# Performance work log

Hardware: AMD Instinct MI355X
Metric: run time of the kernel (lower is better)

## Reference

```python
import jax, jax.numpy as jnp
import numpy as np

B = 2048   # batch of manifold points
D = 16     # manifold_dim


def setup_inputs() -> dict:
    key = jax.random.key(0)
    k1, k2 = jax.random.split(key)
    a = jax.random.normal(k1, (B, D, D), dtype=jnp.float32)
    # SPD, well-conditioned metric so the inverse in scalar_curvature is stable
    metric = jnp.einsum('bij,bkj->bik', a, a) / D + jnp.eye(D, dtype=jnp.float32)
    christoffel = jax.random.normal(k2, (B, D, D, D), dtype=jnp.float32) * 0.1
    return {"metric": metric, "christoffel": christoffel}


def reference(metric, christoffel):
    # --- riemann_curvature (fully vectorized; replaces dim^4 python loops) ---
    # torch.roll(christoffel[:, i, j, x], 1, dims=0) - christoffel[:, i, j, x]
    dG = jnp.roll(christoffel, 1, axis=0) - christoffel          # [B, i, j, x]
    partial_k = dG[:, :, :, None, :]                             # broadcast over k, indexed by l
    partial_l = dG[:, :, :, :, None]                             # broadcast over l, indexed by k
    # conn1[b,i,j,k,l] = sum_m Gamma[b,i,m,k] * Gamma[b,m,j,l]
    conn1 = jnp.einsum('bimk,bmjl->bijkl', christoffel, christoffel)
    # conn2[b,i,j,k,l] = sum_m Gamma[b,i,m,l] * Gamma[b,m,j,k]
    conn2 = jnp.einsum('biml,bmjk->bijkl', christoffel, christoffel)
    riemann = partial_k - partial_l + conn1 - conn2              # [B, D, D, D, D]

    # --- ricci_curvature: contraction 'bkikj->bij' ---
    ricci = jnp.einsum('bkikj->bij', riemann)                    # [B, D, D]

    # --- scalar_curvature: R = g^{ij} Ric_{ij} ---
    metric_inv = jnp.linalg.inv(metric)
    scalar = jnp.einsum('bij,bij->b', ricci, metric_inv)         # [B]
    return scalar
```

## Files before the change

kernel.cpp:

```cpp
#include <hip/hip_runtime.h>
#include <hip/hip_bf16.h>

#define NB 2048

typedef __attribute__((ext_vector_type(8))) short bf16x8;
typedef __attribute__((ext_vector_type(4))) float f32x4;

__device__ __forceinline__ float qget(const float4& q, int c) {
    return c == 0 ? q.x : c == 1 ? q.y : c == 2 ? q.z : q.w;
}

template<int CTRL>
__device__ __forceinline__ float dpp_mov(float x) {
    union { float f; int i; } u; u.f = x;
    u.i = __builtin_amdgcn_mov_dpp(u.i, CTRL, 0xf, 0xf, true);
    return u.f;
}
#define ROWSUM16(x) { x += dpp_mov<0x111>(x); x += dpp_mov<0x112>(x); \
                      x += dpp_mov<0x114>(x); x += dpp_mov<0x118>(x); }

#define GJ_STEP(K) { \
    constexpr int kq = (K) >> 2, kc = (K) & 3; \
    float akc = (kc == 0) ? a0 : (kc == 1) ? a1 : (kc == 2) ? a2 : a3; \
    union { float f; int i; } ua_, uf_, up_; \
    ua_.f = akc; \
    up_.i = __builtin_amdgcn_readlane(ua_.i, ((K) << 2) | kq); \
    uf_.i = __builtin_amdgcn_mov_dpp(ua_.i, kq * 0x55, 0xf, 0xf, 0); \
    float pv = up_.f; \
    float f  = uf_.f; \
    float q0 = __shfl(a0, ((K) << 2) | gq2); \
    float q1 = __shfl(a1, ((K) << 2) | gq2); \
    float q2 = __shfl(a2, ((K) << 2) | gq2); \
    float q3 = __shfl(a3, ((K) << 2) | gq2); \
    float pinv = 1.0f / pv; \
    bool piv = (gi == (K)); \
    float r0 = q0 * pinv, r1 = q1 * pinv, r2 = q2 * pinv, r3 = q3 * pinv; \
    a0 = piv ? r0 : fmaf(-f, r0, a0); \
    a1 = piv ? r1 : fmaf(-f, r1, a1); \
    a2 = piv ? r2 : fmaf(-f, r2, a2); \
    a3 = piv ? r3 : fmaf(-f, r3, a3); \
    float colv = piv ? pinv : -f * pinv; \
    bool fix = (gq2 == kq); \
    if      (kc == 0) a0 = fix ? colv : a0; \
    else if (kc == 1) a1 = fix ? colv : a1; \
    else if (kc == 2) a2 = fix ? colv : a2; \
    else              a3 = fix ? colv : a3; \
}

__global__ __launch_bounds__(256, 6)
void curvature_kernel(const float* __restrict__ metric,
                      const float* __restrict__ gamma,
                      float* __restrict__ out)
{
    const int bid = blockIdx.x;
    const int b = ((bid & 7) << 8) | (bid >> 3);
    const int t = threadIdx.x;
    const int wv = t >> 6, lane = t & 63;
    const int ku = t >> 4, iu = t & 15;
    const int r16 = lane & 15, hi = lane >> 4;
    const int gjw = b & 3;

    __shared__ alignas(16) unsigned short XA[16][264];
    __shared__ alignas(16) float MINV[16][20];
    __shared__ alignas(16) float TT[16][20];
    __shared__ float red[4];

    const float* Gc = gamma + ((size_t)b << 12);
    const float* Gp = gamma + ((size_t)((b + NB - 1) & (NB - 1)) << 12);
    const float4* gc4 = (const float4*)(Gc + (t << 4));
    const float4* gp4 = (const float4*)(Gp + (t << 4));
    const bool isGJ = (wv == gjw);

    float4 g0 = gc4[0], g1 = gc4[1], g2 = gc4[2], g3 = gc4[3];
    float4 mrow = {0.f, 0.f, 0.f, 0.f};
    if (isGJ) mrow = ((const float4*)(metric + ((size_t)b << 8)))[lane];

    float gku;
    {
        float4 gq[4] = {g0, g1, g2, g3};
        gku = g0.x;
        #pragma unroll
        for (int k = 1; k < 16; ++k) {
            float v = qget(gq[k >> 2], k & 3);
            gku = (ku == k) ? v : gku;
        }
    }

    if (isGJ) {
        const int gi = lane >> 2, gq2 = lane & 3;
        float a0 = mrow.x, a1 = mrow.y, a2 = mrow.z, a3 = mrow.w;
        GJ_STEP(0)  GJ_STEP(1)  GJ_STEP(2)  GJ_STEP(3)
        GJ_STEP(4)  GJ_STEP(5)  GJ_STEP(6)  GJ_STEP(7)
        GJ_STEP(8)  GJ_STEP(9)  GJ_STEP(10) GJ_STEP(11)
        GJ_STEP(12) GJ_STEP(13) GJ_STEP(14) GJ_STEP(15)
        MINV[gi][4*gq2 + 0] = a0;
        MINV[gi][4*gq2 + 1] = a1;
        MINV[gi][4*gq2 + 2] = a2;
        MINV[gi][4*gq2 + 3] = a3;
    }

    {
        float4 gq[4] = {g0, g1, g2, g3};
        unsigned yp[8];
        #pragma unroll
        for (int q = 0; q < 8; ++q) {
            union { __hip_bfloat162 h; unsigned u; } cv;
            cv.h = __float22bfloat162_rn(
                make_float2(qget(gq[q >> 1], (q & 1) * 2),
                            qget(gq[q >> 1], (q & 1) * 2 + 1)));
            yp[q] = cv.u;
        }
        uint4* xd = (uint4*)&XA[iu][ku << 4];
        xd[0] = make_uint4(yp[0], yp[1], yp[2], yp[3]);
        xd[1] = make_uint4(yp[4], yp[5], yp[6], yp[7]);
    }
    TT[iu][ku] = gku;
    __syncthreads();

    float4 m0, m1, m2, m3;
    {
        const float4* mv = (const float4*)&MINV[iu][0];
        m0 = mv[0]; m1 = mv[1]; m2 = mv[2]; m3 = mv[3];
    }

    f32x4 acc = {0.f, 0.f, 0.f, 0.f};
    #pragma unroll
    for (int s = 0; s < 2; ++s) {
        const int S = 2 * wv + s;
        bf16x8 av = *(const bf16x8*)&XA[r16][(S << 5) + (hi << 3)];
        const int brow = 2 * S + (hi >> 1);
        const int cbase = ((hi & 1) << 7) + r16;
        bf16x8 bv;
        #pragma unroll
        for (int e = 0; e < 8; ++e)
            bv[e] = (short)XA[brow][cbase + (e << 4)];
        acc = __builtin_amdgcn_mfma_f32_16x16x32_bf16(av, bv, acc, 0, 0, 0);
    }

    float pd = 0.f, pku = 0.f;
    {
        float4 v0 = gp4[0], v1 = gp4[1], v2 = gp4[2], v3 = gp4[3];
        float4 vq[4] = {v0, v1, v2, v3};
        #pragma unroll
        for (int k = 0; k < 16; ++k) {
            float v = qget(vq[k >> 2], k & 3);
            float m = qget((k < 4) ? m0 : (k < 8) ? m1 : (k < 12) ? m2 : m3, k & 3);
            pd = fmaf(v, m, pd);
            pku = (ku == k) ? v : pku;
        }
    }

    float qd = 0.f, R = 0.f;
    {
        float4 gq[4] = {g0, g1, g2, g3};
        #pragma unroll
        for (int k = 0; k < 16; ++k) {
            float m = qget((k < 4) ? m0 : (k < 8) ? m1 : (k < 12) ? m2 : m3, k & 3);
            qd = fmaf(qget(gq[k >> 2], k & 3), m, qd);
            R += m;
        }
    }

    float tsum = TT[ku][iu];
    float qsum = qd;
    ROWSUM16(tsum)
    ROWSUM16(qsum)

    float dt = pku - gku;
    float4 mq = (hi == 0) ? m0 : (hi == 1) ? m1 : (hi == 2) ? m2 : m3;
    float t4c = acc[0] * mq.x + acc[1] * mq.y + acc[2] * mq.z + acc[3] * mq.w;

    float s = pd - dt * R - t4c;
    if (iu == 15) s = fmaf(tsum - 1.0f, qsum, s);

    ROWSUM16(s)
    s += dpp_mov<0x142>(s);
    s += dpp_mov<0x143>(s);
    if (lane == 63) red[wv] = s;
    __syncthreads();
    if (t == 0) out[b] = (red[0] + red[1]) + (red[2] + red[3]);
}

extern "C" void kernel_launch(void* const* d_in, const int* in_sizes, int n_in,
                              void* d_out, int out_size, void* d_ws, size_t ws_size,
                              hipStream_t stream) {
    const float* metric = (const float*)d_in[0];
    const float* gamma  = (const float*)d_in[1];
    float* out = (float*)d_out;
    curvature_kernel<<<NB, 256, 0, stream>>>(metric, gamma, out);
}
```

Measured before the change: 12.46 us.

## Scatter roll-derivative term to neighbor batch via atomics instead of reloading previous christoffel

Each block no longer reads the previous batch's 16 KB christoffel slice. Instead it inverts the next batch's metric in a second wavefront and computes that batch's derivative contribution from its own christoffel data, adding both partial sums to the output with atomicAdd. The output must now be zeroed with an extra memset launch. This removes half of the gamma traffic, at the cost of a second Gauss-Jordan inversion per block, atomic writes, and a memset that falls inside the timed region.

```diff
diff --git a/kernel.cpp b/kernel.cpp
--- a/kernel.cpp
+++ b/kernel.cpp
@@ -54,26 +54,28 @@
 {
     const int bid = blockIdx.x;
     const int b = ((bid & 7) << 8) | (bid >> 3);
+    const int bn = (b + 1) & (NB - 1);
     const int t = threadIdx.x;
     const int wv = t >> 6, lane = t & 63;
     const int ku = t >> 4, iu = t & 15;
     const int r16 = lane & 15, hi = lane >> 4;
-    const int gjw = b & 3;
+    const int gjw  = b & 3;
+    const int gjw2 = (gjw + 1) & 3;
 
     __shared__ alignas(16) unsigned short XA[16][264];
     __shared__ alignas(16) float MINV[16][20];
+    __shared__ alignas(16) float MINVN[16][20];
     __shared__ alignas(16) float TT[16][20];
-    __shared__ float red[4];
+    __shared__ float red[4], red2[4];
 
     const float* Gc = gamma + ((size_t)b << 12);
-    const float* Gp = gamma + ((size_t)((b + NB - 1) & (NB - 1)) << 12);
     const float4* gc4 = (const float4*)(Gc + (t << 4));
-    const float4* gp4 = (const float4*)(Gp + (t << 4));
-    const bool isGJ = (wv == gjw);
+    const bool isGJ1 = (wv == gjw), isGJ2 = (wv == gjw2);
 
     float4 g0 = gc4[0], g1 = gc4[1], g2 = gc4[2], g3 = gc4[3];
     float4 mrow = {0.f, 0.f, 0.f, 0.f};
-    if (isGJ) mrow = ((const float4*)(metric + ((size_t)b << 8)))[lane];
+    if (isGJ1) mrow = ((const float4*)(metric + ((size_t)b  << 8)))[lane];
+    if (isGJ2) mrow = ((const float4*)(metric + ((size_t)bn << 8)))[lane];
 
     float gku;
     {
@@ -86,17 +88,18 @@
         }
     }
 
-    if (isGJ) {
+    if (isGJ1 || isGJ2) {
+        float (*MDST)[20] = isGJ1 ? MINV : MINVN;
         const int gi = lane >> 2, gq2 = lane & 3;
         float a0 = mrow.x, a1 = mrow.y, a2 = mrow.z, a3 = mrow.w;
         GJ_STEP(0)  GJ_STEP(1)  GJ_STEP(2)  GJ_STEP(3)
         GJ_STEP(4)  GJ_STEP(5)  GJ_STEP(6)  GJ_STEP(7)
         GJ_STEP(8)  GJ_STEP(9)  GJ_STEP(10) GJ_STEP(11)
         GJ_STEP(12) GJ_STEP(13) GJ_STEP(14) GJ_STEP(15)
-        MINV[gi][4*gq2 + 0] = a0;
-        MINV[gi][4*gq2 + 1] = a1;
-        MINV[gi][4*gq2 + 2] = a2;
-        MINV[gi][4*gq2 + 3] = a3;
+        MDST[gi][4*gq2 + 0] = a0;
+        MDST[gi][4*gq2 + 1] = a1;
+        MDST[gi][4*gq2 + 2] = a2;
+        MDST[gi][4*gq2 + 3] = a3;
     }
 
     {
@@ -117,10 +120,12 @@
     TT[iu][ku] = gku;
     __syncthreads();
 
-    float4 m0, m1, m2, m3;
+    float4 m0, m1, m2, m3, n0, n1, n2, n3;
     {
         const float4* mv = (const float4*)&MINV[iu][0];
         m0 = mv[0]; m1 = mv[1]; m2 = mv[2]; m3 = mv[3];
+        const float4* nv = (const float4*)&MINVN[iu][0];
+        n0 = nv[0]; n1 = nv[1]; n2 = nv[2]; n3 = nv[3];
     }
 
     f32x4 acc = {0.f, 0.f, 0.f, 0.f};
@@ -137,27 +142,18 @@
         acc = __builtin_amdgcn_mfma_f32_16x16x32_bf16(av, bv, acc, 0, 0, 0);
     }
 
-    float pd = 0.f, pku = 0.f;
-    {
-        float4 v0 = gp4[0], v1 = gp4[1], v2 = gp4[2], v3 = gp4[3];
-        float4 vq[4] = {v0, v1, v2, v3};
-        #pragma unroll
-        for (int k = 0; k < 16; ++k) {
-            float v = qget(vq[k >> 2], k & 3);
-            float m = qget((k < 4) ? m0 : (k < 8) ? m1 : (k < 12) ? m2 : m3, k & 3);
-            pd = fmaf(v, m, pd);
-            pku = (ku == k) ? v : pku;
-        }
-    }
-
-    float qd = 0.f, R = 0.f;
+    float qd = 0.f, R = 0.f, pn = 0.f, Rn = 0.f;
     {
         float4 gq[4] = {g0, g1, g2, g3};
         #pragma unroll
         for (int k = 0; k < 16; ++k) {
+            float v = qget(gq[k >> 2], k & 3);
             float m = qget((k < 4) ? m0 : (k < 8) ? m1 : (k < 12) ? m2 : m3, k & 3);
-            qd = fmaf(qget(gq[k >> 2], k & 3), m, qd);
+            float n = qget((k < 4) ? n0 : (k < 8) ? n1 : (k < 12) ? n2 : n3, k & 3);
+            qd = fmaf(v, m, qd);
+            pn = fmaf(v, n, pn);
             R += m;
+            Rn += n;
         }
     }
 
@@ -166,19 +162,23 @@
     ROWSUM16(tsum)
     ROWSUM16(qsum)
 
-    float dt = pku - gku;
     float4 mq = (hi == 0) ? m0 : (hi == 1) ? m1 : (hi == 2) ? m2 : m3;
     float t4c = acc[0] * mq.x + acc[1] * mq.y + acc[2] * mq.z + acc[3] * mq.w;
 
-    float s = pd - dt * R - t4c;
+    float s = fmaf(gku, R, -t4c);
     if (iu == 15) s = fmaf(tsum - 1.0f, qsum, s);
+    float s2 = fmaf(-gku, Rn, pn);
 
     ROWSUM16(s)
-    s += dpp_mov<0x142>(s);
-    s += dpp_mov<0x143>(s);
-    if (lane == 63) red[wv] = s;
+    s += dpp_mov<0x142>(s);   s += dpp_mov<0x143>(s);
+    ROWSUM16(s2)
+    s2 += dpp_mov<0x142>(s2); s2 += dpp_mov<0x143>(s2);
+    if (lane == 63) { red[wv] = s; red2[wv] = s2; }
     __syncthreads();
-    if (t == 0) out[b] = (red[0] + red[1]) + (red[2] + red[3]);
+    if (t == 0) {
+        atomicAdd(&out[b],  (red[0]  + red[1])  + (red[2]  + red[3]));
+        atomicAdd(&out[bn], (red2[0] + red2[1]) + (red2[2] + red2[3]));
+    }
 }
 
 extern "C" void kernel_launch(void* const* d_in, const int* in_sizes, int n_in,
@@ -187,5 +187,6 @@
     const float* metric = (const float*)d_in[0];
     const float* gamma  = (const float*)d_in[1];
     float* out = (float*)d_out;
+    hipMemsetAsync(out, 0, (size_t)out_size * sizeof(float), stream);
     curvature_kernel<<<NB, 256, 0, stream>>>(metric, gamma, out);
 }
```

Result: slower. 19.67 us (+57.9%).
